# Performance work log

Measured on AMD Instinct MI355X. Metric: run time of the kernel, lower is better.

Reference implementation:

```python
import jax, jax.numpy as jnp
import numpy as np

S, B, E = 3072, 1, 1024          # total tokens, batch, embed_dim
H, HK, D = 16, 8, 64              # num_heads, num_kv_heads, head_dim
SEQ_BOUNDS = [0, 1024, 2048, 3072]  # cu_seqlens: 3 images of 1024 tokens
NEG_INF = -1e9


def setup_inputs() -> dict:
    key = jax.random.key(0)
    ks = jax.random.split(key, 5)
    x = jax.random.normal(ks[0], (S, B, E), jnp.float32)
    qkv_w = jax.random.normal(ks[1], ((H + 2 * HK) * D, E), jnp.float32) * 0.02
    qkv_b = jax.random.normal(ks[2], ((H + 2 * HK) * D,), jnp.float32) * 0.02
    proj_w = jax.random.normal(ks[3], (E, H * D), jnp.float32) * 0.02
    proj_b = jax.random.normal(ks[4], (E,), jnp.float32) * 0.02
    # rotary tables: positions restart within each image window
    pos = (jnp.arange(S) % 1024).astype(jnp.float32)
    inv_freq = 1.0 / (10000.0 ** (jnp.arange(D // 2, dtype=jnp.float32) / (D // 2)))
    ang = pos[:, None] * inv_freq[None, :]            # (S, D/2)
    return {
        "x": x,
        "cu_seqlens": jnp.array(SEQ_BOUNDS, jnp.int32),
        "rotary_cos": jnp.cos(ang),
        "rotary_sin": jnp.sin(ang),
        "qkv_w": qkv_w,
        "qkv_b": qkv_b,
        "proj_w": proj_w,
        "proj_b": proj_b,
        "max_seqlen": 1024,
    }


def _apply_rope(t, cos, sin):
    # t: (b, s, h, d); cos/sin: (s, d/2) -- flash-attn non-interleaved style
    d2 = cos.shape[-1]
    t1, t2 = t[..., :d2], t[..., d2:]
    c = cos[None, :, None, :]
    s = sin[None, :, None, :]
    return jnp.concatenate([t1 * c - t2 * s, t1 * s + t2 * c], axis=-1)


def reference(x, cu_seqlens, rotary_cos, rotary_sin, qkv_w, qkv_b, proj_w, proj_b, max_seqlen):
    s_len, b = x.shape[0], x.shape[1]
    # fused QKV projection
    qkv = x @ qkv_w.T + qkv_b                          # (s, b, (H+2HK)*D)
    qkv = qkv.reshape(s_len, b, H + 2 * HK, D)
    q = jnp.transpose(qkv[:, :, :H, :], (1, 0, 2, 3))             # (b, s, H, D)
    k = jnp.transpose(qkv[:, :, H:H + HK, :], (1, 0, 2, 3))       # (b, s, HK, D)
    v = jnp.transpose(qkv[:, :, H + HK:, :], (1, 0, 2, 3))        # (b, s, HK, D)
    # rotary embedding on q and k
    q = _apply_rope(q, rotary_cos, rotary_sin)
    k = _apply_rope(k, rotary_cos, rotary_sin)
    # GQA: repeat kv heads
    k = jnp.repeat(k, H // HK, axis=2)                 # (b, s, H, D)
    v = jnp.repeat(v, H // HK, axis=2)
    # varlen (block-diagonal) attention via segment-id mask
    seg = jnp.searchsorted(cu_seqlens, jnp.arange(s_len, dtype=jnp.int32), side="right")
    mask = seg[:, None] == seg[None, :]                # (s, s)
    scale = D ** -0.5
    scores = jnp.einsum("bshd,bthd->bhst", q, k) * scale  # (b, H, s, s)
    scores = jnp.where(mask[None, None, :, :], scores, NEG_INF)
    attn = jax.nn.softmax(scores, axis=-1)
    ctx = jnp.einsum("bhst,bthd->bshd", attn, v)        # (b, s, H, D)
    # rearrange 'b s h d -> s b (h d)' and output projection
    ctx = jnp.transpose(ctx, (1, 0, 2, 3)).reshape(s_len, b, H * D)
    return ctx @ proj_w.T + proj_b                      # (s, b, E)
```

## Files before the change

### kernel.cpp

```cpp
#include <hip/hip_runtime.h>
#include <cstdint>
#include <cstddef>

#define S_LEN 3072
#define E_DIM 1024
#define NH 16
#define NKV 8
#define HD 64
#define NQKV 2048
#define SEG 1024

typedef __attribute__((ext_vector_type(8))) short bf16x8;
typedef __attribute__((ext_vector_type(4))) float f32x4;
typedef __attribute__((ext_vector_type(4))) float ff4;
typedef unsigned short u16;

__device__ __forceinline__ u16 f2bf(float f) {
    unsigned u = __float_as_uint(f);
    u += 0x7fffu + ((u >> 16) & 1u);
    return (u16)(u >> 16);
}

__device__ __forceinline__ void gld16(const void* g, u16* l) {
    __builtin_amdgcn_global_load_lds(
        (const __attribute__((address_space(1))) unsigned*)g,
        (__attribute__((address_space(3))) unsigned*)l, 16, 0, 0);
}

__global__ __launch_bounds__(256) void k_cast(
    const float* __restrict__ x, const float* __restrict__ w, const float* __restrict__ pw,
    u16* __restrict__ xb, u16* __restrict__ wb, u16* __restrict__ pwb)
{
    const int n1 = (S_LEN * E_DIM) / 4, n2 = (NQKV * E_DIM) / 4, n3 = (E_DIM * E_DIM) / 4;
    const int total = n1 + n2 + n3;
    for (int i = blockIdx.x * 256 + threadIdx.x; i < total; i += gridDim.x * 256) {
        const float* s; u16* d; int j;
        if (i < n1)           { s = x;  d = xb;  j = i; }
        else if (i < n1 + n2) { s = w;  d = wb;  j = i - n1; }
        else                  { s = pw; d = pwb; j = i - n1 - n2; }
        ff4 v = *(const ff4*)&s[(size_t)j * 4];
        unsigned lo = (unsigned)f2bf(v.x) | ((unsigned)f2bf(v.y) << 16);
        unsigned hi = (unsigned)f2bf(v.z) | ((unsigned)f2bf(v.w) << 16);
        uint2 pk; pk.x = lo; pk.y = hi;
        *(uint2*)&d[(size_t)j * 4] = pk;
    }
}

__global__ __launch_bounds__(256) void k_qkv(
    const u16* __restrict__ xb, const u16* __restrict__ wb,
    const float* __restrict__ bias, const float* __restrict__ rc, const float* __restrict__ rs,
    u16* __restrict__ qb, u16* __restrict__ kb, u16* __restrict__ vb)
{
    __shared__ u16 smA[64 * 64];
    __shared__ u16 smB[128 * 64];
    const int tid = threadIdx.x;
    const int wv = tid >> 6, ln = tid & 63;
    const int s0 = blockIdx.x * 64;
    const int o0 = blockIdx.y * 128;
    const int wr = wv >> 1, wc = wv & 1;
    const int col = ln & 15, lg = ln >> 4;

    f32x4 acc[2][4] = {};

    for (int kt = 0; kt < E_DIM / 64; ++kt) {
        const int k0 = kt * 64;
        #pragma unroll
        for (int i = 0; i < 2; ++i) {
            int c = i * 256 + tid;
            int row = c >> 3, sl = c & 7;
            int gs = (sl ^ (row & 7)) << 3;
            gld16(&xb[(size_t)(s0 + row) * E_DIM + k0 + gs], &smA[(i * 256 + wv * 64) * 8]);
        }
        #pragma unroll
        for (int i = 0; i < 4; ++i) {
            int c = i * 256 + tid;
            int row = c >> 3, sl = c & 7;
            int gs = (sl ^ (row & 7)) << 3;
            gld16(&wb[(size_t)(o0 + row) * E_DIM + k0 + gs], &smB[(i * 256 + wv * 64) * 8]);
        }
        __syncthreads();
        #pragma unroll
        for (int ks = 0; ks < 2; ++ks) {
            bf16x8 a[2], b[4];
            #pragma unroll
            for (int mi = 0; mi < 2; ++mi) {
                int row = wr * 32 + mi * 16 + col;
                int sl = (ks * 4 + lg) ^ (row & 7);
                a[mi] = *(const bf16x8*)&smA[row * 64 + sl * 8];
            }
            #pragma unroll
            for (int ni = 0; ni < 4; ++ni) {
                int row = wc * 64 + ni * 16 + col;
                int sl = (ks * 4 + lg) ^ (row & 7);
                b[ni] = *(const bf16x8*)&smB[row * 64 + sl * 8];
            }
            #pragma unroll
            for (int mi = 0; mi < 2; ++mi)
                #pragma unroll
                for (int ni = 0; ni < 4; ++ni)
                    acc[mi][ni] = __builtin_amdgcn_mfma_f32_16x16x32_bf16(a[mi], b[ni], acc[mi][ni], 0, 0, 0);
        }
        __syncthreads();
    }

    const int ocol0 = o0 + wc * 64;
    const int head = ocol0 >> 6;
    #pragma unroll
    for (int ni = 0; ni < 4; ++ni) {
        float bv = bias[ocol0 + ni * 16 + col];
        #pragma unroll
        for (int mi = 0; mi < 2; ++mi)
            #pragma unroll
            for (int r = 0; r < 4; ++r)
                acc[mi][ni][r] += bv;
    }
    if (head < NH + NKV) {
        #pragma unroll
        for (int mi = 0; mi < 2; ++mi)
            #pragma unroll
            for (int r = 0; r < 4; ++r) {
                int s = s0 + wr * 32 + mi * 16 + lg * 4 + r;
                #pragma unroll
                for (int ni = 0; ni < 2; ++ni) {
                    int d2 = ni * 16 + col;
                    float c = rc[s * 32 + d2], sn = rs[s * 32 + d2];
                    float t1 = acc[mi][ni][r], t2 = acc[mi][ni + 2][r];
                    acc[mi][ni][r]     = t1 * c - t2 * sn;
                    acc[mi][ni + 2][r] = t1 * sn + t2 * c;
                }
            }
    }
    #pragma unroll
    for (int mi = 0; mi < 2; ++mi)
        #pragma unroll
        for (int r = 0; r < 4; ++r) {
            int s = s0 + wr * 32 + mi * 16 + lg * 4 + r;
            #pragma unroll
            for (int ni = 0; ni < 4; ++ni) {
                int d = ni * 16 + col;
                u16 hv = f2bf(acc[mi][ni][r]);
                if (head < NH)
                    qb[((size_t)head * S_LEN + s) * HD + d] = hv;
                else if (head < NH + NKV)
                    kb[((size_t)(head - NH) * S_LEN + s) * HD + d] = hv;
                else
                    vb[((size_t)(head - NH - NKV) * HD + d) * S_LEN + s] = hv;
            }
        }
}

__global__ __launch_bounds__(256) void k_attn(
    const u16* __restrict__ qb, const u16* __restrict__ kb, const u16* __restrict__ vb,
    u16* __restrict__ cb)
{
    __shared__ u16 smK[64 * 64];
    __shared__ u16 smV[64 * 64];
    __shared__ u16 smP[4 * 16 * 64];
    const int tid = threadIdx.x;
    const int wv = tid >> 6, ln = tid & 63;
    const int h = blockIdx.y, kvh = h >> 1;
    const int s0 = blockIdx.x * 64;
    const int seg0 = s0 & ~(SEG - 1);
    const int col = ln & 15, lg = ln >> 4;

    bf16x8 qf[2];
    #pragma unroll
    for (int ks = 0; ks < 2; ++ks)
        qf[ks] = *(const bf16x8*)&qb[((size_t)h * S_LEN + s0 + wv * 16 + col) * HD + ks * 32 + lg * 8];

    f32x4 oacc[4] = {};
    float l[4] = {0.f, 0.f, 0.f, 0.f};
    u16* myP = &smP[wv * 16 * 64];

    for (int kt = 0; kt < SEG / 64; ++kt) {
        const int t0 = seg0 + kt * 64;
        #pragma unroll
        for (int i = 0; i < 2; ++i) {
            int c = i * 256 + tid; int row = c >> 3, sl = c & 7; int gs = (sl ^ (row & 7)) << 3;
            gld16(&kb[((size_t)kvh * S_LEN + t0 + row) * HD + gs], &smK[(i * 256 + wv * 64) * 8]);
        }
        #pragma unroll
        for (int i = 0; i < 2; ++i) {
            int c = i * 256 + tid; int row = c >> 3, sl = c & 7; int gs = (sl ^ (row & 7)) << 3;
            gld16(&vb[((size_t)kvh * HD + row) * S_LEN + t0 + gs], &smV[(i * 256 + wv * 64) * 8]);
        }
        __syncthreads();

        f32x4 sacc[4] = {};
        #pragma unroll
        for (int ks = 0; ks < 2; ++ks) {
            bf16x8 kf[4];
            #pragma unroll
            for (int ni = 0; ni < 4; ++ni) {
                int row = ni * 16 + col;
                int sl = (ks * 4 + lg) ^ (row & 7);
                kf[ni] = *(const bf16x8*)&smK[row * 64 + sl * 8];
            }
            #pragma unroll
            for (int ni = 0; ni < 4; ++ni)
                sacc[ni] = __builtin_amdgcn_mfma_f32_16x16x32_bf16(qf[ks], kf[ni], sacc[ni], 0, 0, 0);
        }

        float rsum[4] = {0.f, 0.f, 0.f, 0.f};
        #pragma unroll
        for (int ni = 0; ni < 4; ++ni)
            #pragma unroll
            for (int r = 0; r < 4; ++r) {
                float p = __expf(sacc[ni][r] * 0.125f);
                sacc[ni][r] = p;
                rsum[r] += p;
            }
        #pragma unroll
        for (int r = 0; r < 4; ++r) {
            float v = rsum[r];
            v += __shfl_xor(v, 1); v += __shfl_xor(v, 2);
            v += __shfl_xor(v, 4); v += __shfl_xor(v, 8);
            l[r] += v;
        }

        #pragma unroll
        for (int ni = 0; ni < 4; ++ni)
            #pragma unroll
            for (int r = 0; r < 4; ++r) {
                int row = lg * 4 + r;
                int t = ni * 16 + col;
                int b = (t >> 3) ^ (row & 7);
                myP[row * 64 + b * 8 + (t & 7)] = f2bf(sacc[ni][r]);
            }

        #pragma unroll
        for (int ks = 0; ks < 2; ++ks) {
            bf16x8 pf, vf[4];
            {
                int row = col;
                int sl = (ks * 4 + lg) ^ (row & 7);
                pf = *(const bf16x8*)&myP[row * 64 + sl * 8];
            }
            #pragma unroll
            for (int ni = 0; ni < 4; ++ni) {
                int row = ni * 16 + col;
                int sl = (ks * 4 + lg) ^ (row & 7);
                vf[ni] = *(const bf16x8*)&smV[row * 64 + sl * 8];
            }
            #pragma unroll
            for (int ni = 0; ni < 4; ++ni)
                oacc[ni] = __builtin_amdgcn_mfma_f32_16x16x32_bf16(pf, vf[ni], oacc[ni], 0, 0, 0);
        }
        __syncthreads();
    }

    #pragma unroll
    for (int r = 0; r < 4; ++r) {
        int s = s0 + wv * 16 + lg * 4 + r;
        float inv = 1.f / l[r];
        #pragma unroll
        for (int ni = 0; ni < 4; ++ni) {
            int d = ni * 16 + col;
            cb[(size_t)s * E_DIM + h * HD + d] = f2bf(oacc[ni][r] * inv);
        }
    }
}

__global__ __launch_bounds__(256) void k_proj(
    const u16* __restrict__ cb, const u16* __restrict__ pwb,
    const float* __restrict__ bias, float* __restrict__ out)
{
    __shared__ u16 smA[64 * 64];
    __shared__ u16 smB[64 * 64];
    const int tid = threadIdx.x;
    const int wv = tid >> 6, ln = tid & 63;
    const int s0 = blockIdx.x * 64, o0 = blockIdx.y * 64;
    const int wr = wv >> 1, wc = wv & 1;
    const int col = ln & 15, lg = ln >> 4;

    f32x4 acc[2][2] = {};

    for (int kt = 0; kt < E_DIM / 64; ++kt) {
        const int k0 = kt * 64;
        #pragma unroll
        for (int i = 0; i < 2; ++i) {
            int c = i * 256 + tid; int row = c >> 3, sl = c & 7; int gs = (sl ^ (row & 7)) << 3;
            gld16(&cb[(size_t)(s0 + row) * E_DIM + k0 + gs], &smA[(i * 256 + wv * 64) * 8]);
        }
        #pragma unroll
        for (int i = 0; i < 2; ++i) {
            int c = i * 256 + tid; int row = c >> 3, sl = c & 7; int gs = (sl ^ (row & 7)) << 3;
            gld16(&pwb[(size_t)(o0 + row) * E_DIM + k0 + gs], &smB[(i * 256 + wv * 64) * 8]);
        }
        __syncthreads();
        #pragma unroll
        for (int ks = 0; ks < 2; ++ks) {
            bf16x8 a[2], b[2];
            #pragma unroll
            for (int mi = 0; mi < 2; ++mi) {
                int row = wr * 32 + mi * 16 + col;
                int sl = (ks * 4 + lg) ^ (row & 7);
                a[mi] = *(const bf16x8*)&smA[row * 64 + sl * 8];
            }
            #pragma unroll
            for (int ni = 0; ni < 2; ++ni) {
                int row = wc * 32 + ni * 16 + col;
                int sl = (ks * 4 + lg) ^ (row & 7);
                b[ni] = *(const bf16x8*)&smB[row * 64 + sl * 8];
            }
            #pragma unroll
            for (int mi = 0; mi < 2; ++mi)
                #pragma unroll
                for (int ni = 0; ni < 2; ++ni)
                    acc[mi][ni] = __builtin_amdgcn_mfma_f32_16x16x32_bf16(a[mi], b[ni], acc[mi][ni], 0, 0, 0);
        }
        __syncthreads();
    }

    #pragma unroll
    for (int mi = 0; mi < 2; ++mi)
        #pragma unroll
        for (int r = 0; r < 4; ++r) {
            int s = s0 + wr * 32 + mi * 16 + lg * 4 + r;
            #pragma unroll
            for (int ni = 0; ni < 2; ++ni) {
                int o = o0 + wc * 32 + ni * 16 + col;
                out[(size_t)s * E_DIM + o] = acc[mi][ni][r] + bias[o];
            }
        }
}

extern "C" void kernel_launch(void* const* d_in, const int* in_sizes, int n_in,
                              void* d_out, int out_size, void* d_ws, size_t ws_size,
                              hipStream_t stream) {
    const float* x      = (const float*)d_in[0];
    const float* rc     = (const float*)d_in[2];
    const float* rs     = (const float*)d_in[3];
    const float* qkv_w  = (const float*)d_in[4];
    const float* qkv_b  = (const float*)d_in[5];
    const float* proj_w = (const float*)d_in[6];
    const float* proj_b = (const float*)d_in[7];
    float* out = (float*)d_out;

    u16* ws  = (u16*)d_ws;
    u16* xb  = ws;
    u16* wb  = xb  + (size_t)S_LEN * E_DIM;
    u16* pwb = wb  + (size_t)NQKV * E_DIM;
    u16* qb  = pwb + (size_t)E_DIM * E_DIM;
    u16* kb  = qb  + (size_t)NH * S_LEN * HD;
    u16* vb  = kb  + (size_t)NKV * S_LEN * HD;
    u16* cb  = vb  + (size_t)NKV * S_LEN * HD;

    k_cast<<<1536, 256, 0, stream>>>(x, qkv_w, proj_w, xb, wb, pwb);
    k_qkv <<<dim3(48, 16), 256, 0, stream>>>(xb, wb, qkv_b, rc, rs, qb, kb, vb);
    k_attn<<<dim3(48, 16), 256, 0, stream>>>(qb, kb, vb, cb);
    k_proj<<<dim3(48, 16), 256, 0, stream>>>(cb, proj_w ? pwb : pwb, proj_b, out);
}
```

Measured before the change: 156.1 us.

## Enlarge tiles in QKV, attention and projection kernels; fold softmax scale into Q

Doubles the row tile to 128 in the QKV GEMM, the attention kernel (each wave now handles 32 query rows) and the output projection (also 128 output columns), so each K/V or weight tile loaded into LDS is reused across more rows. The 1/sqrt(D) scale is folded into Q at QKV-epilogue time, and V stores are packed into 4-element vector writes instead of scalar ones. Grids shrink to 384 blocks for QKV and attention and 192 for projection, which on a 256-CU part risks leaving CUs underused, and register pressure rises with the larger accumulators.

```diff
diff --git a/kernel.cpp b/kernel.cpp
--- a/kernel.cpp
+++ b/kernel.cpp
@@ -13,6 +13,7 @@
 typedef __attribute__((ext_vector_type(8))) short bf16x8;
 typedef __attribute__((ext_vector_type(4))) float f32x4;
 typedef __attribute__((ext_vector_type(4))) float ff4;
+typedef __attribute__((ext_vector_type(4))) short s16x4;
 typedef unsigned short u16;
 
 __device__ __forceinline__ u16 f2bf(float f) {
@@ -51,21 +52,21 @@
     const float* __restrict__ bias, const float* __restrict__ rc, const float* __restrict__ rs,
     u16* __restrict__ qb, u16* __restrict__ kb, u16* __restrict__ vb)
 {
-    __shared__ u16 smA[64 * 64];
+    __shared__ u16 smA[128 * 64];
     __shared__ u16 smB[128 * 64];
     const int tid = threadIdx.x;
     const int wv = tid >> 6, ln = tid & 63;
-    const int s0 = blockIdx.x * 64;
+    const int s0 = blockIdx.x * 128;
     const int o0 = blockIdx.y * 128;
     const int wr = wv >> 1, wc = wv & 1;
     const int col = ln & 15, lg = ln >> 4;
 
-    f32x4 acc[2][4] = {};
+    f32x4 acc[4][4] = {};
 
     for (int kt = 0; kt < E_DIM / 64; ++kt) {
         const int k0 = kt * 64;
         #pragma unroll
-        for (int i = 0; i < 2; ++i) {
+        for (int i = 0; i < 4; ++i) {
             int c = i * 256 + tid;
             int row = c >> 3, sl = c & 7;
             int gs = (sl ^ (row & 7)) << 3;
@@ -81,10 +82,10 @@
         __syncthreads();
         #pragma unroll
         for (int ks = 0; ks < 2; ++ks) {
-            bf16x8 a[2], b[4];
-            #pragma unroll
-            for (int mi = 0; mi < 2; ++mi) {
-                int row = wr * 32 + mi * 16 + col;
+            bf16x8 a[4], b[4];
+            #pragma unroll
+            for (int mi = 0; mi < 4; ++mi) {
+                int row = wr * 64 + mi * 16 + col;
                 int sl = (ks * 4 + lg) ^ (row & 7);
                 a[mi] = *(const bf16x8*)&smA[row * 64 + sl * 8];
             }
@@ -95,7 +96,7 @@
                 b[ni] = *(const bf16x8*)&smB[row * 64 + sl * 8];
             }
             #pragma unroll
-            for (int mi = 0; mi < 2; ++mi)
+            for (int mi = 0; mi < 4; ++mi)
                 #pragma unroll
                 for (int ni = 0; ni < 4; ++ni)
                     acc[mi][ni] = __builtin_amdgcn_mfma_f32_16x16x32_bf16(a[mi], b[ni], acc[mi][ni], 0, 0, 0);
@@ -109,17 +110,17 @@
     for (int ni = 0; ni < 4; ++ni) {
         float bv = bias[ocol0 + ni * 16 + col];
         #pragma unroll
-        for (int mi = 0; mi < 2; ++mi)
+        for (int mi = 0; mi < 4; ++mi)
             #pragma unroll
             for (int r = 0; r < 4; ++r)
                 acc[mi][ni][r] += bv;
     }
     if (head < NH + NKV) {
         #pragma unroll
-        for (int mi = 0; mi < 2; ++mi)
+        for (int mi = 0; mi < 4; ++mi)
             #pragma unroll
             for (int r = 0; r < 4; ++r) {
-                int s = s0 + wr * 32 + mi * 16 + lg * 4 + r;
+                int s = s0 + wr * 64 + mi * 16 + lg * 4 + r;
                 #pragma unroll
                 for (int ni = 0; ni < 2; ++ni) {
                     int d2 = ni * 16 + col;
@@ -130,23 +131,42 @@
                 }
             }
     }
-    #pragma unroll
-    for (int mi = 0; mi < 2; ++mi)
-        #pragma unroll
-        for (int r = 0; r < 4; ++r) {
-            int s = s0 + wr * 32 + mi * 16 + lg * 4 + r;
+    if (head < NH) {
+        #pragma unroll
+        for (int mi = 0; mi < 4; ++mi)
+            #pragma unroll
+            for (int ni = 0; ni < 4; ++ni)
+                #pragma unroll
+                for (int r = 0; r < 4; ++r)
+                    acc[mi][ni][r] *= 0.125f;
+    }
+    if (head < NH + NKV) {
+        u16* dst; int hh;
+        if (head < NH) { dst = qb; hh = head; } else { dst = kb; hh = head - NH; }
+        #pragma unroll
+        for (int mi = 0; mi < 4; ++mi)
+            #pragma unroll
+            for (int r = 0; r < 4; ++r) {
+                int s = s0 + wr * 64 + mi * 16 + lg * 4 + r;
+                #pragma unroll
+                for (int ni = 0; ni < 4; ++ni)
+                    dst[((size_t)hh * S_LEN + s) * HD + ni * 16 + col] = f2bf(acc[mi][ni][r]);
+            }
+    } else {
+        int hh = head - NH - NKV;
+        #pragma unroll
+        for (int mi = 0; mi < 4; ++mi) {
+            int sb = s0 + wr * 64 + mi * 16 + lg * 4;
             #pragma unroll
             for (int ni = 0; ni < 4; ++ni) {
                 int d = ni * 16 + col;
-                u16 hv = f2bf(acc[mi][ni][r]);
-                if (head < NH)
-                    qb[((size_t)head * S_LEN + s) * HD + d] = hv;
-                else if (head < NH + NKV)
-                    kb[((size_t)(head - NH) * S_LEN + s) * HD + d] = hv;
-                else
-                    vb[((size_t)(head - NH - NKV) * HD + d) * S_LEN + s] = hv;
-            }
-        }
+                s16x4 pk;
+                #pragma unroll
+                for (int r = 0; r < 4; ++r) pk[r] = (short)f2bf(acc[mi][ni][r]);
+                *(s16x4*)&vb[((size_t)hh * HD + d) * S_LEN + sb] = pk;
+            }
+        }
+    }
 }
 
 __global__ __launch_bounds__(256) void k_attn(
@@ -155,22 +175,24 @@
 {
     __shared__ u16 smK[64 * 64];
     __shared__ u16 smV[64 * 64];
-    __shared__ u16 smP[4 * 16 * 64];
+    __shared__ u16 smP[4 * 32 * 64];
     const int tid = threadIdx.x;
     const int wv = tid >> 6, ln = tid & 63;
     const int h = blockIdx.y, kvh = h >> 1;
-    const int s0 = blockIdx.x * 64;
+    const int s0 = blockIdx.x * 128;
     const int seg0 = s0 & ~(SEG - 1);
     const int col = ln & 15, lg = ln >> 4;
 
-    bf16x8 qf[2];
+    bf16x8 qf[2][2];
     #pragma unroll
-    for (int ks = 0; ks < 2; ++ks)
-        qf[ks] = *(const bf16x8*)&qb[((size_t)h * S_LEN + s0 + wv * 16 + col) * HD + ks * 32 + lg * 8];
-
-    f32x4 oacc[4] = {};
-    float l[4] = {0.f, 0.f, 0.f, 0.f};
-    u16* myP = &smP[wv * 16 * 64];
+    for (int mi = 0; mi < 2; ++mi)
+        #pragma unroll
+        for (int ks = 0; ks < 2; ++ks)
+            qf[mi][ks] = *(const bf16x8*)&qb[((size_t)h * S_LEN + s0 + wv * 32 + mi * 16 + col) * HD + ks * 32 + lg * 8];
+
+    f32x4 oacc[2][4] = {};
+    float l[2][4] = {};
+    u16* myP = &smP[wv * 32 * 64];
 
     for (int kt = 0; kt < SEG / 64; ++kt) {
         const int t0 = seg0 + kt * 64;
@@ -186,7 +208,7 @@
         }
         __syncthreads();
 
-        f32x4 sacc[4] = {};
+        f32x4 sacc[2][4] = {};
         #pragma unroll
         for (int ks = 0; ks < 2; ++ks) {
             bf16x8 kf[4];
@@ -197,129 +219,136 @@
                 kf[ni] = *(const bf16x8*)&smK[row * 64 + sl * 8];
             }
             #pragma unroll
+            for (int mi = 0; mi < 2; ++mi)
+                #pragma unroll
+                for (int ni = 0; ni < 4; ++ni)
+                    sacc[mi][ni] = __builtin_amdgcn_mfma_f32_16x16x32_bf16(qf[mi][ks], kf[ni], sacc[mi][ni], 0, 0, 0);
+        }
+
+        #pragma unroll
+        for (int mi = 0; mi < 2; ++mi) {
+            float rsum[4] = {0.f, 0.f, 0.f, 0.f};
+            #pragma unroll
             for (int ni = 0; ni < 4; ++ni)
-                sacc[ni] = __builtin_amdgcn_mfma_f32_16x16x32_bf16(qf[ks], kf[ni], sacc[ni], 0, 0, 0);
-        }
-
-        float rsum[4] = {0.f, 0.f, 0.f, 0.f};
-        #pragma unroll
-        for (int ni = 0; ni < 4; ++ni)
+                #pragma unroll
+                for (int r = 0; r < 4; ++r) {
+                    float p = __expf(sacc[mi][ni][r]);
+                    sacc[mi][ni][r] = p;
+                    rsum[r] += p;
+                }
             #pragma unroll
             for (int r = 0; r < 4; ++r) {
-                float p = __expf(sacc[ni][r] * 0.125f);
-                sacc[ni][r] = p;
-                rsum[r] += p;
-            }
+                float v = rsum[r];
+                v += __shfl_xor(v, 1); v += __shfl_xor(v, 2);
+                v += __shfl_xor(v, 4); v += __shfl_xor(v, 8);
+                l[mi][r] += v;
+            }
+            #pragma unroll
+            for (int ni = 0; ni < 4; ++ni)
+                #pragma unroll
+                for (int r = 0; r < 4; ++r) {
+                    int row = mi * 16 + lg * 4 + r;
+                    int t = ni * 16 + col;
+                    int b = (t >> 3) ^ (row & 7);
+                    myP[row * 64 + b * 8 + (t & 7)] = f2bf(sacc[mi][ni][r]);
+                }
+        }
+
+        #pragma unroll
+        for (int ks = 0; ks < 2; ++ks) {
+            bf16x8 pf[2], vf[4];
+            #pragma unroll
+            for (int mi = 0; mi < 2; ++mi) {
+                int row = mi * 16 + col;
+                int sl = (ks * 4 + lg) ^ (row & 7);
+                pf[mi] = *(const bf16x8*)&myP[row * 64 + sl * 8];
+            }
+            #pragma unroll
+            for (int ni = 0; ni < 4; ++ni) {
+                int row = ni * 16 + col;
+                int sl = (ks * 4 + lg) ^ (row & 7);
+                vf[ni] = *(const bf16x8*)&smV[row * 64 + sl * 8];
+            }
+            #pragma unroll
+            for (int mi = 0; mi < 2; ++mi)
+                #pragma unroll
+                for (int ni = 0; ni < 4; ++ni)
+                    oacc[mi][ni] = __builtin_amdgcn_mfma_f32_16x16x32_bf16(pf[mi], vf[ni], oacc[mi][ni], 0, 0, 0);
+        }
+        __syncthreads();
+    }
+
+    #pragma unroll
+    for (int mi = 0; mi < 2; ++mi)
         #pragma unroll
         for (int r = 0; r < 4; ++r) {
-            float v = rsum[r];
-            v += __shfl_xor(v, 1); v += __shfl_xor(v, 2);
-            v += __shfl_xor(v, 4); v += __shfl_xor(v, 8);
-            l[r] += v;
-        }
-
-        #pragma unroll
-        for (int ni = 0; ni < 4; ++ni)
-            #pragma unroll
-            for (int r = 0; r < 4; ++r) {
-                int row = lg * 4 + r;
-                int t = ni * 16 + col;
-                int b = (t >> 3) ^ (row & 7);
-                myP[row * 64 + b * 8 + (t & 7)] = f2bf(sacc[ni][r]);
-            }
-
-        #pragma unroll
-        for (int ks = 0; ks < 2; ++ks) {
-            bf16x8 pf, vf[4];
-            {
-                int row = col;
-                int sl = (ks * 4 + lg) ^ (row & 7);
-                pf = *(const bf16x8*)&myP[row * 64 + sl * 8];
-            }
-            #pragma unroll
-            for (int ni = 0; ni < 4; ++ni) {
-                int row = ni * 16 + col;
-                int sl = (ks * 4 + lg) ^ (row & 7);
-                vf[ni] = *(const bf16x8*)&smV[row * 64 + sl * 8];
-            }
+            int s = s0 + wv * 32 + mi * 16 + lg * 4 + r;
+            float inv = 1.f / l[mi][r];
             #pragma unroll
             for (int ni = 0; ni < 4; ++ni)
-                oacc[ni] = __builtin_amdgcn_mfma_f32_16x16x32_bf16(pf, vf[ni], oacc[ni], 0, 0, 0);
-        }
-        __syncthreads();
-    }
-
-    #pragma unroll
-    for (int r = 0; r < 4; ++r) {
-        int s = s0 + wv * 16 + lg * 4 + r;
-        float inv = 1.f / l[r];
-        #pragma unroll
-        for (int ni = 0; ni < 4; ++ni) {
-            int d = ni * 16 + col;
-            cb[(size_t)s * E_DIM + h * HD + d] = f2bf(oacc[ni][r] * inv);
-        }
-    }
+                cb[(size_t)s * E_DIM + h * HD + ni * 16 + col] = f2bf(oacc[mi][ni][r] * inv);
+        }
 }
 
 __global__ __launch_bounds__(256) void k_proj(
     const u16* __restrict__ cb, const u16* __restrict__ pwb,
     const float* __restrict__ bias, float* __restrict__ out)
 {
-    __shared__ u16 smA[64 * 64];
-    __shared__ u16 smB[64 * 64];
+    __shared__ u16 smA[128 * 64];
+    __shared__ u16 smB[128 * 64];
     const int tid = threadIdx.x;
     const int wv = tid >> 6, ln = tid & 63;
-    const int s0 = blockIdx.x * 64, o0 = blockIdx.y * 64;
+    const int s0 = blockIdx.x * 128, o0 = blockIdx.y * 128;
     const int wr = wv >> 1, wc = wv & 1;
     const int col = ln & 15, lg = ln >> 4;
 
-    f32x4 acc[2][2] = {};
+    f32x4 acc[4][4] = {};
 
     for (int kt = 0; kt < E_DIM / 64; ++kt) {
         const int k0 = kt * 64;
         #pragma unroll
-        for (int i = 0; i < 2; ++i) {
+        for (int i = 0; i < 4; ++i) {
             int c = i * 256 + tid; int row = c >> 3, sl = c & 7; int gs = (sl ^ (row & 7)) << 3;
             gld16(&cb[(size_t)(s0 + row) * E_DIM + k0 + gs], &smA[(i * 256 + wv * 64) * 8]);
         }
         #pragma unroll
-        for (int i = 0; i < 2; ++i) {
+        for (int i = 0; i < 4; ++i) {
             int c = i * 256 + tid; int row = c >> 3, sl = c & 7; int gs = (sl ^ (row & 7)) << 3;
             gld16(&pwb[(size_t)(o0 + row) * E_DIM + k0 + gs], &smB[(i * 256 + wv * 64) * 8]);
         }
         __syncthreads();
         #pragma unroll
         for (int ks = 0; ks < 2; ++ks) {
-            bf16x8 a[2], b[2];
-            #pragma unroll
-            for (int mi = 0; mi < 2; ++mi) {
-                int row = wr * 32 + mi * 16 + col;
+            bf16x8 a[4], b[4];
+            #pragma unroll
+            for (int mi = 0; mi < 4; ++mi) {
+                int row = wr * 64 + mi * 16 + col;
                 int sl = (ks * 4 + lg) ^ (row & 7);
                 a[mi] = *(const bf16x8*)&smA[row * 64 + sl * 8];
             }
             #pragma unroll
-            for (int ni = 0; ni < 2; ++ni) {
-                int row = wc * 32 + ni * 16 + col;
+            for (int ni = 0; ni < 4; ++ni) {
+                int row = wc * 64 + ni * 16 + col;
                 int sl = (ks * 4 + lg) ^ (row & 7);
                 b[ni] = *(const bf16x8*)&smB[row * 64 + sl * 8];
             }
             #pragma unroll
-            for (int mi = 0; mi < 2; ++mi)
-                #pragma unroll
-                for (int ni = 0; ni < 2; ++ni)
+            for (int mi = 0; mi < 4; ++mi)
+                #pragma unroll
+                for (int ni = 0; ni < 4; ++ni)
                     acc[mi][ni] = __builtin_amdgcn_mfma_f32_16x16x32_bf16(a[mi], b[ni], acc[mi][ni], 0, 0, 0);
         }
         __syncthreads();
     }
 
     #pragma unroll
-    for (int mi = 0; mi < 2; ++mi)
+    for (int mi = 0; mi < 4; ++mi)
         #pragma unroll
         for (int r = 0; r < 4; ++r) {
-            int s = s0 + wr * 32 + mi * 16 + lg * 4 + r;
-            #pragma unroll
-            for (int ni = 0; ni < 2; ++ni) {
-                int o = o0 + wc * 32 + ni * 16 + col;
+            int s = s0 + wr * 64 + mi * 16 + lg * 4 + r;
+            #pragma unroll
+            for (int ni = 0; ni < 4; ++ni) {
+                int o = o0 + wc * 64 + ni * 16 + col;
                 out[(size_t)s * E_DIM + o] = acc[mi][ni][r] + bias[o];
             }
         }
@@ -347,7 +376,7 @@
     u16* cb  = vb  + (size_t)NKV * S_LEN * HD;
 
     k_cast<<<1536, 256, 0, stream>>>(x, qkv_w, proj_w, xb, wb, pwb);
-    k_qkv <<<dim3(48, 16), 256, 0, stream>>>(xb, wb, qkv_b, rc, rs, qb, kb, vb);
-    k_attn<<<dim3(48, 16), 256, 0, stream>>>(qb, kb, vb, cb);
-    k_proj<<<dim3(48, 16), 256, 0, stream>>>(cb, proj_w ? pwb : pwb, proj_b, out);
-}
+    k_qkv <<<dim3(24, 16), 256, 0, stream>>>(xb, wb, qkv_b, rc, rs, qb, kb, vb);
+    k_attn<<<dim3(24, 16), 256, 0, stream>>>(qb, kb, vb, cb);
+    k_proj<<<dim3(24, 8),  256, 0, stream>>>(cb, pwb, proj_b, out);
+}
```

After: 173.3 us. 1.11x slower.

## Prescale Q by log2e/sqrt(d), use exp2, defer row-sum reduction, vectorize V stores

Applied to the files above, without the earlier changes.

The QKV kernel now multiplies Q by scale*log2(e) before the bf16 cast, so the attention kernel can call the hardware exp2 directly with no per-element multiply. The per-tile cross-lane shuffle reduction of the softmax row sums is moved out of the key loop and done once at the end. V transposed stores are packed into 4-element vector writes. The attention still has no max subtraction, and prescaling Q before bf16 rounding slightly changes numerics.

```diff
diff --git a/kernel.cpp b/kernel.cpp
--- a/kernel.cpp
+++ b/kernel.cpp
@@ -13,7 +13,10 @@
 typedef __attribute__((ext_vector_type(8))) short bf16x8;
 typedef __attribute__((ext_vector_type(4))) float f32x4;
 typedef __attribute__((ext_vector_type(4))) float ff4;
+typedef __attribute__((ext_vector_type(4))) short s16x4;
 typedef unsigned short u16;
+
+#define QSCALE 0.1803368801111204f
 
 __device__ __forceinline__ u16 f2bf(float f) {
     unsigned u = __float_as_uint(f);
@@ -130,23 +133,42 @@
                 }
             }
     }
-    #pragma unroll
-    for (int mi = 0; mi < 2; ++mi)
-        #pragma unroll
-        for (int r = 0; r < 4; ++r) {
-            int s = s0 + wr * 32 + mi * 16 + lg * 4 + r;
+    if (head < NH) {
+        #pragma unroll
+        for (int mi = 0; mi < 2; ++mi)
+            #pragma unroll
+            for (int ni = 0; ni < 4; ++ni)
+                #pragma unroll
+                for (int r = 0; r < 4; ++r)
+                    acc[mi][ni][r] *= QSCALE;
+    }
+    if (head < NH + NKV) {
+        u16* dst; int hh;
+        if (head < NH) { dst = qb; hh = head; } else { dst = kb; hh = head - NH; }
+        #pragma unroll
+        for (int mi = 0; mi < 2; ++mi)
+            #pragma unroll
+            for (int r = 0; r < 4; ++r) {
+                int s = s0 + wr * 32 + mi * 16 + lg * 4 + r;
+                #pragma unroll
+                for (int ni = 0; ni < 4; ++ni)
+                    dst[((size_t)hh * S_LEN + s) * HD + ni * 16 + col] = f2bf(acc[mi][ni][r]);
+            }
+    } else {
+        int hh = head - NH - NKV;
+        #pragma unroll
+        for (int mi = 0; mi < 2; ++mi) {
+            int sb = s0 + wr * 32 + mi * 16 + lg * 4;
             #pragma unroll
             for (int ni = 0; ni < 4; ++ni) {
                 int d = ni * 16 + col;
-                u16 hv = f2bf(acc[mi][ni][r]);
-                if (head < NH)
-                    qb[((size_t)head * S_LEN + s) * HD + d] = hv;
-                else if (head < NH + NKV)
-                    kb[((size_t)(head - NH) * S_LEN + s) * HD + d] = hv;
-                else
-                    vb[((size_t)(head - NH - NKV) * HD + d) * S_LEN + s] = hv;
-            }
-        }
+                s16x4 pk;
+                #pragma unroll
+                for (int r = 0; r < 4; ++r) pk[r] = (short)f2bf(acc[mi][ni][r]);
+                *(s16x4*)&vb[((size_t)hh * HD + d) * S_LEN + sb] = pk;
+            }
+        }
+    }
 }
 
 __global__ __launch_bounds__(256) void k_attn(
@@ -169,7 +191,7 @@
         qf[ks] = *(const bf16x8*)&qb[((size_t)h * S_LEN + s0 + wv * 16 + col) * HD + ks * 32 + lg * 8];
 
     f32x4 oacc[4] = {};
-    float l[4] = {0.f, 0.f, 0.f, 0.f};
+    float lsum[4] = {0.f, 0.f, 0.f, 0.f};
     u16* myP = &smP[wv * 16 * 64];
 
     for (int kt = 0; kt < SEG / 64; ++kt) {
@@ -201,22 +223,14 @@
                 sacc[ni] = __builtin_amdgcn_mfma_f32_16x16x32_bf16(qf[ks], kf[ni], sacc[ni], 0, 0, 0);
         }
 
-        float rsum[4] = {0.f, 0.f, 0.f, 0.f};
         #pragma unroll
         for (int ni = 0; ni < 4; ++ni)
             #pragma unroll
             for (int r = 0; r < 4; ++r) {
-                float p = __expf(sacc[ni][r] * 0.125f);
+                float p = __builtin_amdgcn_exp2f(sacc[ni][r]);
                 sacc[ni][r] = p;
-                rsum[r] += p;
-            }
-        #pragma unroll
-        for (int r = 0; r < 4; ++r) {
-            float v = rsum[r];
-            v += __shfl_xor(v, 1); v += __shfl_xor(v, 2);
-            v += __shfl_xor(v, 4); v += __shfl_xor(v, 8);
-            l[r] += v;
-        }
+                lsum[r] += p;
+            }
 
         #pragma unroll
         for (int ni = 0; ni < 4; ++ni)
@@ -251,8 +265,16 @@
 
     #pragma unroll
     for (int r = 0; r < 4; ++r) {
+        float v = lsum[r];
+        v += __shfl_xor(v, 1); v += __shfl_xor(v, 2);
+        v += __shfl_xor(v, 4); v += __shfl_xor(v, 8);
+        lsum[r] = v;
+    }
+
+    #pragma unroll
+    for (int r = 0; r < 4; ++r) {
         int s = s0 + wv * 16 + lg * 4 + r;
-        float inv = 1.f / l[r];
+        float inv = 1.f / lsum[r];
         #pragma unroll
         for (int ni = 0; ni < 4; ++ni) {
             int d = ni * 16 + col;
@@ -349,5 +371,5 @@
     k_cast<<<1536, 256, 0, stream>>>(x, qkv_w, proj_w, xb, wb, pwb);
     k_qkv <<<dim3(48, 16), 256, 0, stream>>>(xb, wb, qkv_b, rc, rs, qb, kb, vb);
     k_attn<<<dim3(48, 16), 256, 0, stream>>>(qb, kb, vb, cb);
-    k_proj<<<dim3(48, 16), 256, 0, stream>>>(cb, proj_w ? pwb : pwb, proj_b, out);
-}
+    k_proj<<<dim3(48, 16), 256, 0, stream>>>(cb, pwb, proj_b, out);
+}
```

Result: faster. 144.9 us (-7.2%).
